# Optimization experiments

Hardware: AMD Instinct MI355X
Metric: run time of the kernel (lower is better)

## Reference

```python
import jax, jax.numpy as jnp
import numpy as np

B, S, D, H, F = 2, 2048, 1024, 16, 4096
HD = D // H
NEG_INF = jnp.float32(-1e30)


def layer_norm(x, gamma, beta, eps=1e-6):
    mu = jnp.mean(x, axis=-1, keepdims=True)
    var = jnp.mean(jnp.square(x - mu), axis=-1, keepdims=True)
    return (x - mu) * jax.lax.rsqrt(var + eps) * gamma + beta


def setup_inputs() -> dict:
    key = jax.random.key(0)
    ks = jax.random.split(key, 8)
    d = np.sqrt(float(D))
    dx_up = np.sqrt(6.0 / (D + F))
    dx_dn = np.sqrt(6.0 / (F + D))
    return {
        "x_embeds": jax.random.normal(ks[0], (B, S, D), dtype=jnp.float32),
        "tokens": jax.random.randint(ks[1], (B, S), 0, 128, dtype=jnp.int32),
        "KQV": jax.random.uniform(ks[2], (D, 3 * D), jnp.float32, -1 / d, 1 / d),
        "WO": jax.random.uniform(ks[3], (D, D), jnp.float32, -1 / d, 1 / d),
        "W_up": jax.random.uniform(ks[4], (D, F), jnp.float32, -dx_up, dx_up),
        "b_up": jnp.zeros((F,), jnp.float32),
        "W_down": jax.random.uniform(ks[5], (F, D), jnp.float32, -dx_dn, dx_dn),
        "b_down": jnp.zeros((D,), jnp.float32),
        "ln1_g": jnp.ones((D,), jnp.float32),
        "ln1_b": jnp.zeros((D,), jnp.float32),
        "ln2_g": jnp.ones((D,), jnp.float32),
        "ln2_b": jnp.zeros((D,), jnp.float32),
        "start_token_id": 1,
    }


def reference(x_embeds, tokens, KQV, WO, W_up, b_up, W_down, b_down,
              ln1_g, ln1_b, ln2_g, ln2_b, start_token_id):
    b, s = x_embeds.shape[0], x_embeds.shape[1]
    # --- attention ---
    x_kqv = jnp.einsum("bsd,de->bse", x_embeds, KQV)          # [B,S,3D]
    x_kqv = x_kqv.reshape(b, s, H, 3, HD)
    k = x_kqv[:, :, :, 0, :]   # [B,S,H,HD]
    q = x_kqv[:, :, :, 1, :]
    v = x_kqv[:, :, :, 2, :]
    inner = jnp.einsum("bqhd,bkhd->bhqk", q, k)               # [B,H,S,S]
    # causal mask
    causal = jnp.tril(jnp.ones((s, s), dtype=bool))           # [S,S]
    # block-diagonal document mask from start tokens
    seg = jnp.cumsum((tokens == start_token_id).astype(jnp.int32), axis=1)  # [B,S]
    same_seg = seg[:, :, None] == seg[:, None, :]             # [B,S,S]
    mask = causal[None, None] & same_seg[:, None]             # [B,1->H,S,S]
    inner = jnp.where(mask, inner, NEG_INF)
    dk = jnp.sqrt(jnp.float32(HD))
    WA = jax.nn.softmax(inner / dk, axis=-1)
    head_outs = jnp.einsum("bhqk,bkhd->bqhd", WA, v)          # [B,S,H,HD]
    out = head_outs.reshape(b, s, D) @ WO
    out = layer_norm(out, ln1_g, ln1_b)
    x = out + x_embeds
    # --- ffnn ---
    h = jax.nn.relu(x @ W_up + b_up)
    out = h @ W_down + b_down
    out = layer_norm(out, ln2_g, ln2_b)
    return out + x
```

## Files before the change

kernel.cpp:

```cpp
#include <hip/hip_runtime.h>

typedef unsigned short u16;
typedef unsigned int u32;
typedef __bf16 bf16_t;
typedef bf16_t bf16x8 __attribute__((ext_vector_type(8)));
typedef u16 u16x8 __attribute__((ext_vector_type(8)));
typedef float f32x4 __attribute__((ext_vector_type(4)));

__device__ __forceinline__ float bf2f(u16 u) {
    union { float f; unsigned i; } c; c.i = ((unsigned)u) << 16; return c.f;
}
__device__ __forceinline__ u16 f2bf(float f) {
    return __builtin_bit_cast(u16, (bf16_t)f);
}
__device__ __forceinline__ f32x4 mfma16(bf16x8 a, bf16x8 b, f32x4 c) {
    return __builtin_amdgcn_mfma_f32_16x16x32_bf16(a, b, c, 0, 0, 0);
}
__device__ __forceinline__ void gld16(const u16* g, u16* l) {
    __builtin_amdgcn_global_load_lds(
        (const __attribute__((address_space(1))) void*)g,
        (__attribute__((address_space(3))) void*)l, 16, 0, 0);
}

__global__ __launch_bounds__(256)
void cvt_kernel(const float* __restrict__ in, u16* __restrict__ out)
{
    const int i = (blockIdx.x * 256 + threadIdx.x) * 8;
    float4 a = *reinterpret_cast<const float4*>(in + i);
    float4 b = *reinterpret_cast<const float4*>(in + i + 4);
    u16x8 o;
    o[0] = f2bf(a.x); o[1] = f2bf(a.y); o[2] = f2bf(a.z); o[3] = f2bf(a.w);
    o[4] = f2bf(b.x); o[5] = f2bf(b.y); o[6] = f2bf(b.z); o[7] = f2bf(b.w);
    *reinterpret_cast<u16x8*>(out + i) = o;
}

__global__ __launch_bounds__(256)
void cvt_t_kernel(const float* __restrict__ in, u16* __restrict__ out,
                  int K, int N)
{
    __shared__ float tile[32][33];
    const int kb = blockIdx.x * 32, nb = blockIdx.y * 32;
    const int r = threadIdx.x >> 3, c4 = threadIdx.x & 7;
    float4 v = *reinterpret_cast<const float4*>(&in[(size_t)(kb + r) * N + nb + c4 * 4]);
    tile[r][c4 * 4 + 0] = v.x; tile[r][c4 * 4 + 1] = v.y;
    tile[r][c4 * 4 + 2] = v.z; tile[r][c4 * 4 + 3] = v.w;
    __syncthreads();
    ushort4 o;
    o.x = f2bf(tile[c4 * 4 + 0][r]);
    o.y = f2bf(tile[c4 * 4 + 1][r]);
    o.z = f2bf(tile[c4 * 4 + 2][r]);
    o.w = f2bf(tile[c4 * 4 + 3][r]);
    *reinterpret_cast<ushort4*>(&out[(size_t)(nb + r) * K + kb + c4 * 4]) = o;
}

template<int BM, int NSPLIT, bool BIAS, bool RELU, bool QSCALE>
__global__ __launch_bounds__(256)
void gemm_kernel(const u16* __restrict__ A, const u16* __restrict__ Bt,
                 const float* __restrict__ bias, u16* __restrict__ C,
                 int M, int N, int K)
{
    __shared__ u16 As[2][BM][32];
    __shared__ u16 Bs[2][128][32];
    constexpr int AI = BM / 32;
    const int tid  = threadIdx.x;
    const int lane = tid & 63;
    const int wid  = tid >> 6;
    const int wm = wid >> 1, wn = wid & 1;
    const int bm = blockIdx.x, bn = blockIdx.y;
    const int kg = lane >> 4;
    const int lc = lane & 15;
    const int pk = kg ^ (lc & 3);

    f32x4 acc[AI][4];
    #pragma unroll
    for (int i = 0; i < AI; ++i)
        #pragma unroll
        for (int j = 0; j < 4; ++j)
            acc[i][j] = f32x4{0.f, 0.f, 0.f, 0.f};

    const int nk = (K >> 5) / NSPLIT;
    const int kbase = (NSPLIT > 1) ? blockIdx.z * nk : 0;

    auto stage = [&](int kt, int b) {
        int ktg = kbase + kt;
        #pragma unroll
        for (int p = 0; p < BM / 64; ++p) {
            int c = wid * BM + p * 64 + lane;
            int row = c >> 2;
            int ko = ((c & 3) ^ (row & 3)) * 8;
            gld16(A + (size_t)(bm * BM + row) * K + ktg * 32 + ko,
                  &As[b][0][0] + c * 8);
        }
        #pragma unroll
        for (int p = 0; p < 2; ++p) {
            int c = wid * 128 + p * 64 + lane;
            int row = c >> 2;
            int ko = ((c & 3) ^ (row & 3)) * 8;
            gld16(Bt + (size_t)(bn * 128 + row) * K + ktg * 32 + ko,
                  &Bs[b][0][0] + c * 8);
        }
    };

    stage(0, 0);
    __syncthreads();
    for (int kt = 0; kt < nk; ++kt) {
        const int cur = kt & 1;
        if (kt + 1 < nk) stage(kt + 1, cur ^ 1);
        bf16x8 af[AI], bf[4];
        #pragma unroll
        for (int i = 0; i < AI; ++i)
            af[i] = *reinterpret_cast<const bf16x8*>(&As[cur][wm * (BM / 2) + i * 16 + lc][pk * 8]);
        #pragma unroll
        for (int j = 0; j < 4; ++j)
            bf[j] = *reinterpret_cast<const bf16x8*>(&Bs[cur][wn * 64 + j * 16 + lc][pk * 8]);
        #pragma unroll
        for (int j = 0; j < 4; ++j)
            #pragma unroll
            for (int i = 0; i < AI; ++i)
                acc[i][j] = mfma16(af[i], bf[j], acc[i][j]);
        __syncthreads();
    }

    u16* Cp = C + (size_t)((NSPLIT > 1) ? blockIdx.z : 0) * M * N;
    #pragma unroll
    for (int i = 0; i < AI; ++i) {
        #pragma unroll
        for (int j = 0; j < 4; ++j) {
            int col = bn * 128 + wn * 64 + j * 16 + lc;
            float bv = 0.f;
            if (BIAS) bv = bias[col];
            float qs = 1.0f;
            if (QSCALE) {
                u32 cm = (u32)col % 192u;
                if (cm >= 64u && cm < 128u) qs = 0.1803368875f;
            }
            #pragma unroll
            for (int r = 0; r < 4; ++r) {
                int row = bm * BM + wm * (BM / 2) + i * 16 + kg * 4 + r;
                float v = acc[i][j][r] + bv;
                if (RELU) v = v > 0.f ? v : 0.f;
                if (QSCALE) v *= qs;
                Cp[(size_t)row * N + col] = f2bf(v);
            }
        }
    }
}

__global__ __launch_bounds__(256)
void qlo_kernel(const int* __restrict__ tokens, const int* __restrict__ start_id,
                int* __restrict__ qlo)
{
    constexpr int S = 2048;
    __shared__ int part[256];
    __shared__ int pref[256];
    const int b = blockIdx.x, tid = threadIdx.x;
    const int sid = start_id[0];
    const int base = b * S + tid * 8;
    int f[8]; int loc = -1;
    #pragma unroll
    for (int j = 0; j < 8; ++j) {
        f[j] = (tokens[base + j] == sid) ? 1 : 0;
        if (f[j]) loc = tid * 8 + j;
    }
    part[tid] = loc;
    __syncthreads();
    if (tid == 0) {
        int run = -1;
        for (int i = 0; i < 256; ++i) { pref[i] = run; run = max(run, part[i]); }
    }
    __syncthreads();
    int run = pref[tid];
    #pragma unroll
    for (int j = 0; j < 8; ++j) {
        if (f[j]) run = tid * 8 + j;
        qlo[base + j] = max(run, 0);
    }
}

#define MASKVAL -60000.0f
#define MINIT   -30000.0f
__global__ __launch_bounds__(256)
void attn_kernel(const u16* __restrict__ qkv, const int* __restrict__ qloA,
                 u16* __restrict__ attn_out)
{
    constexpr int S = 2048, DQ = 3072;
    __shared__ u16 Ks[64][72];
    __shared__ u16 Vt[64][72];
    __shared__ u16 Pt[4][16][72];
    __shared__ int wm4[4];

    const int tid = threadIdx.x;
    const int lane = tid & 63, w = tid >> 6;
    const int kg = lane >> 4, lc = lane & 15;
    const int qt = blockIdx.x, h = blockIdx.y, b = blockIdx.z;
    const size_t rowbase = (size_t)b * S;
    const int colK = h * 192, colQ = colK + 64, colV = colK + 128;
    const int qrow = qt * 64 + w * 16 + lc;

    bf16x8 qf0, qf1;
    {
        const u16* qp = &qkv[(rowbase + qrow) * DQ + colQ];
        qf0 = *reinterpret_cast<const bf16x8*>(qp + kg * 8);
        qf1 = *reinterpret_cast<const bf16x8*>(qp + 32 + kg * 8);
    }
    const int myqlo = qloA[rowbase + qrow];

    int vmin = myqlo;
    #pragma unroll
    for (int m = 1; m < 16; m <<= 1) vmin = min(vmin, __shfl_xor(vmin, m));
    if (lane == 0) wm4[w] = vmin;
    __syncthreads();
    const int kb0 = min(min(wm4[0], wm4[1]), min(wm4[2], wm4[3])) >> 6;

    float m_ = MINIT, l_ = 0.f;
    f32x4 o[4];
    #pragma unroll
    for (int d = 0; d < 4; ++d) o[d] = f32x4{0.f, 0.f, 0.f, 0.f};

    const int kr = tid >> 3, kc = tid & 7;
    const int rpv = tid >> 3, chv = tid & 7;
    uint4 gk0, gk1, gv0, gv1;

    auto issue = [&](int kb) {
        const size_t base = rowbase + (size_t)kb * 64;
        gk0 = *reinterpret_cast<const uint4*>(&qkv[(base + kr) * DQ + colK + kc * 8]);
        gk1 = *reinterpret_cast<const uint4*>(&qkv[(base + 32 + kr) * DQ + colK + kc * 8]);
        const u16* vp = &qkv[(base + rpv * 2) * DQ + colV + chv * 8];
        gv0 = *reinterpret_cast<const uint4*>(vp);
        gv1 = *reinterpret_cast<const uint4*>(vp + DQ);
    };
    auto write_lds = [&]() {
        *reinterpret_cast<uint4*>(&Ks[kr][kc * 8]) = gk0;
        *reinterpret_cast<uint4*>(&Ks[32 + kr][kc * 8]) = gk1;
        u16x8 va = __builtin_bit_cast(u16x8, gv0);
        u16x8 vb = __builtin_bit_cast(u16x8, gv1);
        const int kp = (rpv * 2) ^ (chv << 3);
        #pragma unroll
        for (int j = 0; j < 8; ++j)
            *reinterpret_cast<u32*>(&Vt[chv * 8 + j][kp]) =
                (u32)va[j] | ((u32)vb[j] << 16);
    };

    issue(kb0);
    for (int kb = kb0; kb <= qt; ++kb) {
        write_lds();
        __syncthreads();
        if (kb < qt) issue(kb + 1);

        f32x4 sT[4];
        #pragma unroll
        for (int ks = 0; ks < 4; ++ks) {
            bf16x8 kf0 = *reinterpret_cast<const bf16x8*>(&Ks[ks * 16 + lc][kg * 8]);
            bf16x8 kf1 = *reinterpret_cast<const bf16x8*>(&Ks[ks * 16 + lc][32 + kg * 8]);
            f32x4 s = f32x4{0.f, 0.f, 0.f, 0.f};
            s = mfma16(kf0, qf0, s);
            s = mfma16(kf1, qf1, s);
            sT[ks] = s;
        }
        const int lo = myqlo - kb * 64, hi = qrow - kb * 64;
        #pragma unroll
        for (int ks = 0; ks < 4; ++ks) {
            #pragma unroll
            for (int r = 0; r < 4; ++r) {
                int kk = ks * 16 + kg * 4 + r;
                bool ok = (kk >= lo) && (kk <= hi);
                sT[ks][r] = ok ? sT[ks][r] : MASKVAL;
            }
        }
        float tm = fmaxf(fmaxf(fmaxf(sT[0][0], sT[0][1]), fmaxf(sT[0][2], sT[0][3])),
                         fmaxf(fmaxf(sT[1][0], sT[1][1]), fmaxf(sT[1][2], sT[1][3])));
        tm = fmaxf(tm, fmaxf(fmaxf(fmaxf(sT[2][0], sT[2][1]), fmaxf(sT[2][2], sT[2][3])),
                             fmaxf(fmaxf(sT[3][0], sT[3][1]), fmaxf(sT[3][2], sT[3][3]))));
        tm = fmaxf(tm, __shfl_xor(tm, 16));
        tm = fmaxf(tm, __shfl_xor(tm, 32));
        float mn = fmaxf(m_, tm);
        float al = exp2f(m_ - mn);
        m_ = mn;
        float ps = 0.f;
        #pragma unroll
        for (int ks = 0; ks < 4; ++ks) {
            ushort4 pw;
            float p0 = exp2f(sT[ks][0] - m_); ps += p0; pw.x = f2bf(p0);
            float p1 = exp2f(sT[ks][1] - m_); ps += p1; pw.y = f2bf(p1);
            float p2 = exp2f(sT[ks][2] - m_); ps += p2; pw.z = f2bf(p2);
            float p3 = exp2f(sT[ks][3] - m_); ps += p3; pw.w = f2bf(p3);
            *reinterpret_cast<ushort4*>(&Pt[w][lc][ks * 16 + kg * 4]) = pw;
        }
        ps += __shfl_xor(ps, 16);
        ps += __shfl_xor(ps, 32);
        l_ = l_ * al + ps;
        float alr[4];
        #pragma unroll
        for (int r = 0; r < 4; ++r) alr[r] = __shfl(al, kg * 4 + r);
        #pragma unroll
        for (int d = 0; d < 4; ++d)
            #pragma unroll
            for (int r = 0; r < 4; ++r) o[d][r] *= alr[r];

        #pragma unroll
        for (int kf = 0; kf < 2; ++kf) {
            bf16x8 pf = *reinterpret_cast<const bf16x8*>(&Pt[w][lc][kf * 32 + kg * 8]);
            #pragma unroll
            for (int d = 0; d < 4; ++d) {
                int vrow = d * 16 + lc;
                int b3 = (kf * 4 + kg) ^ ((vrow >> 3) & 7);
                bf16x8 vf = *reinterpret_cast<const bf16x8*>(&Vt[vrow][b3 * 8]);
                o[d] = mfma16(pf, vf, o[d]);
            }
        }
        __syncthreads();
    }

    float lr[4];
    #pragma unroll
    for (int r = 0; r < 4; ++r) lr[r] = __shfl(l_, kg * 4 + r);
    #pragma unroll
    for (int d = 0; d < 4; ++d)
        #pragma unroll
        for (int r = 0; r < 4; ++r) {
            float v = o[d][r] / fmaxf(lr[r], 1e-20f);
            int qo = qt * 64 + w * 16 + kg * 4 + r;
            attn_out[(rowbase + qo) * 1024 + h * 64 + d * 16 + lc] = f2bf(v);
        }
}

template<bool SPLIT, bool WRITE_BF>
__global__ __launch_bounds__(256)
void ln_kernel(const u16* __restrict__ in, const u16* __restrict__ in2,
               const float* __restrict__ gam, const float* __restrict__ bet,
               const float* res, float* out_f, u16* __restrict__ out_bf)
{
    const int row = blockIdx.x;
    const int tid = threadIdx.x;
    const int lane = tid & 63, w = tid >> 6;
    __shared__ float red1[4], red2[4];

    const size_t base = (size_t)row * 1024 + tid * 4;
    ushort4 xv = *reinterpret_cast<const ushort4*>(in + base);
    float x0 = bf2f(xv.x), x1 = bf2f(xv.y), x2 = bf2f(xv.z), x3 = bf2f(xv.w);
    if constexpr (SPLIT) {
        ushort4 yv = *reinterpret_cast<const ushort4*>(in2 + base);
        x0 += bf2f(yv.x); x1 += bf2f(yv.y); x2 += bf2f(yv.z); x3 += bf2f(yv.w);
    }

    float s = x0 + x1 + x2 + x3;
    #pragma unroll
    for (int m = 1; m < 64; m <<= 1) s += __shfl_xor(s, m);
    if (lane == 0) red1[w] = s;
    __syncthreads();
    float mu = (red1[0] + red1[1] + red1[2] + red1[3]) * (1.0f / 1024.0f);

    float d0 = x0 - mu, d1 = x1 - mu, d2 = x2 - mu, d3 = x3 - mu;
    float q = d0 * d0 + d1 * d1 + d2 * d2 + d3 * d3;
    #pragma unroll
    for (int m = 1; m < 64; m <<= 1) q += __shfl_xor(q, m);
    if (lane == 0) red2[w] = q;
    __syncthreads();
    float var = (red2[0] + red2[1] + red2[2] + red2[3]) * (1.0f / 1024.0f);
    float rs = rsqrtf(var + 1e-6f);

    float dd[4] = {d0, d1, d2, d3};
    #pragma unroll
    for (int e = 0; e < 4; ++e) {
        int col = tid * 4 + e;
        size_t idx = (size_t)row * 1024 + col;
        float y = dd[e] * rs * gam[col] + bet[col];
        float ov = y + res[idx];
        out_f[idx] = ov;
        if constexpr (WRITE_BF) out_bf[idx] = f2bf(ov);
    }
}

extern "C" void kernel_launch(void* const* d_in, const int* in_sizes, int n_in,
                              void* d_out, int out_size, void* d_ws, size_t ws_size,
                              hipStream_t stream)
{
    const float* x_emb = (const float*)d_in[0];
    const int* tokens  = (const int*)d_in[1];
    const float* KQV   = (const float*)d_in[2];
    const float* WO    = (const float*)d_in[3];
    const float* W_up  = (const float*)d_in[4];
    const float* b_up  = (const float*)d_in[5];
    const float* W_dn  = (const float*)d_in[6];
    const float* b_dn  = (const float*)d_in[7];
    const float* g1    = (const float*)d_in[8];
    const float* be1   = (const float*)d_in[9];
    const float* g2    = (const float*)d_in[10];
    const float* be2   = (const float*)d_in[11];
    const int* start   = (const int*)d_in[12];

    char* ws = (char*)d_ws;
    u16* XB     = (u16*)(ws + 0);
    u16* KBt    = (u16*)(ws + 8388608);
    u16* qkv    = (u16*)(ws + 14680064);
    int* qloA   = (int*)(ws + 39845888);
    u16* attn_o = (u16*)(ws + 41943040);
    u16* WOBt   = (u16*)(ws + 8388608);
    u16* cpart  = (u16*)(ws + 16777216);
    u16* x_bf   = (u16*)(ws + 8388608);
    u16* WUBt   = (u16*)(ws + 0);
    u16* hbuf   = (u16*)(ws + 16777216);
    u16* WDBt   = (u16*)(ws + 0);
    u16* t2     = (u16*)(ws + 8388608);
    float* x_f  = (float*)d_out;
    float* outp = (float*)d_out;

    cvt_kernel<<<2048, 256, 0, stream>>>(x_emb, XB);
    cvt_t_kernel<<<dim3(32, 96), 256, 0, stream>>>(KQV, KBt, 1024, 3072);
    qlo_kernel<<<2, 256, 0, stream>>>(tokens, start, qloA);
    gemm_kernel<128, 1, false, false, true><<<dim3(32, 24), 256, 0, stream>>>(XB, KBt, nullptr, qkv, 4096, 3072, 1024);
    cvt_t_kernel<<<dim3(32, 32), 256, 0, stream>>>(WO, WOBt, 1024, 1024);
    attn_kernel<<<dim3(32, 16, 2), 256, 0, stream>>>(qkv, qloA, attn_o);
    gemm_kernel<128, 2, false, false, false><<<dim3(32, 8, 2), 256, 0, stream>>>(attn_o, WOBt, nullptr, cpart, 4096, 1024, 1024);
    ln_kernel<true, true><<<4096, 256, 0, stream>>>(cpart, cpart + 4194304, g1, be1, x_emb, x_f, x_bf);
    cvt_t_kernel<<<dim3(32, 128), 256, 0, stream>>>(W_up, WUBt, 1024, 4096);
    gemm_kernel<128, 1, true, true, false><<<dim3(32, 32), 256, 0, stream>>>(x_bf, WUBt, b_up, hbuf, 4096, 4096, 1024);
    cvt_t_kernel<<<dim3(128, 32), 256, 0, stream>>>(W_dn, WDBt, 4096, 1024);
    gemm_kernel<64, 1, true, false, false><<<dim3(64, 8), 256, 0, stream>>>(hbuf, WDBt, b_dn, t2, 4096, 1024, 4096);
    ln_kernel<false, false><<<4096, 256, 0, stream>>>(t2, nullptr, g2, be2, x_f, outp, nullptr);
}
```

Measured before the change: 252.0 us.

## Split-K the down-projection GEMM and change the LDS swizzle pattern

The down-projection GEMM (K=4096) now uses split-K with 4 or 2 partitions when the workspace allows, writing bf16 partial sums that the final layernorm kernel adds together. The bias is added only in the first split. The LDS XOR swizzle now mixes higher row bits to reduce bank conflicts on the fragment reads. The workspace layout and launch order are rearranged so the W_up conversion runs before the WO GEMM. The trade-off is extra partial-sum memory traffic and bf16 rounding of each partial sum.

```diff
diff --git a/kernel.cpp b/kernel.cpp
--- a/kernel.cpp
+++ b/kernel.cpp
@@ -69,7 +69,7 @@
     const int bm = blockIdx.x, bn = blockIdx.y;
     const int kg = lane >> 4;
     const int lc = lane & 15;
-    const int pk = kg ^ (lc & 3);
+    const int pk = kg ^ ((lc + (lc >> 2)) & 3);
 
     f32x4 acc[AI][4];
     #pragma unroll
@@ -86,17 +86,15 @@
         #pragma unroll
         for (int p = 0; p < BM / 64; ++p) {
             int c = wid * BM + p * 64 + lane;
-            int row = c >> 2;
-            int ko = ((c & 3) ^ (row & 3)) * 8;
-            gld16(A + (size_t)(bm * BM + row) * K + ktg * 32 + ko,
+            int ko = (((c & 3) ^ (((c >> 2) + (c >> 4)) & 3))) * 8;
+            gld16(A + (size_t)(bm * BM + (c >> 2)) * K + ktg * 32 + ko,
                   &As[b][0][0] + c * 8);
         }
         #pragma unroll
         for (int p = 0; p < 2; ++p) {
             int c = wid * 128 + p * 64 + lane;
-            int row = c >> 2;
-            int ko = ((c & 3) ^ (row & 3)) * 8;
-            gld16(Bt + (size_t)(bn * 128 + row) * K + ktg * 32 + ko,
+            int ko = (((c & 3) ^ (((c >> 2) + (c >> 4)) & 3))) * 8;
+            gld16(Bt + (size_t)(bn * 128 + (c >> 2)) * K + ktg * 32 + ko,
                   &Bs[b][0][0] + c * 8);
         }
     };
@@ -122,13 +120,13 @@
     }
 
     u16* Cp = C + (size_t)((NSPLIT > 1) ? blockIdx.z : 0) * M * N;
+    const bool addb = BIAS && (NSPLIT == 1 || blockIdx.z == 0);
     #pragma unroll
     for (int i = 0; i < AI; ++i) {
         #pragma unroll
         for (int j = 0; j < 4; ++j) {
             int col = bn * 128 + wn * 64 + j * 16 + lc;
-            float bv = 0.f;
-            if (BIAS) bv = bias[col];
+            float bv = addb ? bias[col] : 0.f;
             float qs = 1.0f;
             if (QSCALE) {
                 u32 cm = (u32)col % 192u;
@@ -324,11 +322,11 @@
         }
 }
 
-template<bool SPLIT, bool WRITE_BF>
-__global__ __launch_bounds__(256)
-void ln_kernel(const u16* __restrict__ in, const u16* __restrict__ in2,
-               const float* __restrict__ gam, const float* __restrict__ bet,
-               const float* res, float* out_f, u16* __restrict__ out_bf)
+template<int NSPL, bool WRITE_BF>
+__global__ __launch_bounds__(256)
+void ln_kernel(const u16* __restrict__ in, const float* __restrict__ gam,
+               const float* __restrict__ bet, const float* res,
+               float* out_f, u16* __restrict__ out_bf)
 {
     const int row = blockIdx.x;
     const int tid = threadIdx.x;
@@ -336,11 +334,11 @@
     __shared__ float red1[4], red2[4];
 
     const size_t base = (size_t)row * 1024 + tid * 4;
-    ushort4 xv = *reinterpret_cast<const ushort4*>(in + base);
-    float x0 = bf2f(xv.x), x1 = bf2f(xv.y), x2 = bf2f(xv.z), x3 = bf2f(xv.w);
-    if constexpr (SPLIT) {
-        ushort4 yv = *reinterpret_cast<const ushort4*>(in2 + base);
-        x0 += bf2f(yv.x); x1 += bf2f(yv.y); x2 += bf2f(yv.z); x3 += bf2f(yv.w);
+    float x0 = 0.f, x1 = 0.f, x2 = 0.f, x3 = 0.f;
+    #pragma unroll
+    for (int sp = 0; sp < NSPL; ++sp) {
+        ushort4 xv = *reinterpret_cast<const ushort4*>(in + (size_t)sp * 4194304 + base);
+        x0 += bf2f(xv.x); x1 += bf2f(xv.y); x2 += bf2f(xv.z); x3 += bf2f(xv.w);
     }
 
     float s = x0 + x1 + x2 + x3;
@@ -389,19 +387,20 @@
     const float* be2   = (const float*)d_in[11];
     const int* start   = (const int*)d_in[12];
 
+    const size_t MiB = 1048576;
     char* ws = (char*)d_ws;
     u16* XB     = (u16*)(ws + 0);
-    u16* KBt    = (u16*)(ws + 8388608);
-    u16* qkv    = (u16*)(ws + 14680064);
-    int* qloA   = (int*)(ws + 39845888);
-    u16* attn_o = (u16*)(ws + 41943040);
-    u16* WOBt   = (u16*)(ws + 8388608);
-    u16* cpart  = (u16*)(ws + 16777216);
-    u16* x_bf   = (u16*)(ws + 8388608);
-    u16* WUBt   = (u16*)(ws + 0);
-    u16* hbuf   = (u16*)(ws + 16777216);
+    u16* qkv    = (u16*)(ws + 8 * MiB);
+    u16* attn_o = (u16*)(ws + 32 * MiB);
+    u16* KBt    = (u16*)(ws + 40 * MiB);
+    int* qloA   = (int*)(ws + 46 * MiB);
+    u16* WOBt   = (u16*)(ws + 0);
+    u16* cpart  = (u16*)(ws + 8 * MiB);
+    u16* x_bf   = (u16*)(ws + 0);
+    u16* WUBt   = (u16*)(ws + 40 * MiB);
+    u16* hbuf   = (u16*)(ws + 8 * MiB);
     u16* WDBt   = (u16*)(ws + 0);
-    u16* t2     = (u16*)(ws + 8388608);
+    u16* fpart  = (u16*)(ws + 40 * MiB);
     float* x_f  = (float*)d_out;
     float* outp = (float*)d_out;
 
@@ -411,11 +410,19 @@
     gemm_kernel<128, 1, false, false, true><<<dim3(32, 24), 256, 0, stream>>>(XB, KBt, nullptr, qkv, 4096, 3072, 1024);
     cvt_t_kernel<<<dim3(32, 32), 256, 0, stream>>>(WO, WOBt, 1024, 1024);
     attn_kernel<<<dim3(32, 16, 2), 256, 0, stream>>>(qkv, qloA, attn_o);
+    cvt_t_kernel<<<dim3(32, 128), 256, 0, stream>>>(W_up, WUBt, 1024, 4096);
     gemm_kernel<128, 2, false, false, false><<<dim3(32, 8, 2), 256, 0, stream>>>(attn_o, WOBt, nullptr, cpart, 4096, 1024, 1024);
-    ln_kernel<true, true><<<4096, 256, 0, stream>>>(cpart, cpart + 4194304, g1, be1, x_emb, x_f, x_bf);
-    cvt_t_kernel<<<dim3(32, 128), 256, 0, stream>>>(W_up, WUBt, 1024, 4096);
+    ln_kernel<2, true><<<4096, 256, 0, stream>>>(cpart, g1, be1, x_emb, x_f, x_bf);
     gemm_kernel<128, 1, true, true, false><<<dim3(32, 32), 256, 0, stream>>>(x_bf, WUBt, b_up, hbuf, 4096, 4096, 1024);
     cvt_t_kernel<<<dim3(128, 32), 256, 0, stream>>>(W_dn, WDBt, 4096, 1024);
-    gemm_kernel<64, 1, true, false, false><<<dim3(64, 8), 256, 0, stream>>>(hbuf, WDBt, b_dn, t2, 4096, 1024, 4096);
-    ln_kernel<false, false><<<4096, 256, 0, stream>>>(t2, nullptr, g2, be2, x_f, outp, nullptr);
-}
+    if (ws_size >= 72 * MiB) {
+        gemm_kernel<128, 4, true, false, false><<<dim3(32, 8, 4), 256, 0, stream>>>(hbuf, WDBt, b_dn, fpart, 4096, 1024, 4096);
+        ln_kernel<4, false><<<4096, 256, 0, stream>>>(fpart, g2, be2, x_f, outp, nullptr);
+    } else if (ws_size >= 56 * MiB) {
+        gemm_kernel<128, 2, true, false, false><<<dim3(32, 8, 2), 256, 0, stream>>>(hbuf, WDBt, b_dn, fpart, 4096, 1024, 4096);
+        ln_kernel<2, false><<<4096, 256, 0, stream>>>(fpart, g2, be2, x_f, outp, nullptr);
+    } else {
+        gemm_kernel<64, 1, true, false, false><<<dim3(64, 8), 256, 0, stream>>>(hbuf, WDBt, b_dn, fpart, 4096, 1024, 4096);
+        ln_kernel<1, false><<<4096, 256, 0, stream>>>(fpart, g2, be2, x_f, outp, nullptr);
+    }
+}
```

After: 243.1 us. 3.5% less time.
